# Kernel tuning notes

Hardware: AMD Instinct MI355X
Metric: run time of the kernel (lower is better)

The kernel has to match this reference:

```python
import jax, jax.numpy as jnp
import numpy as np

EPS = 1e-5
EXTEND_SCOPE = 1.0

def conv2d(x, w, b, pad):
    out = jax.lax.conv_general_dilated(x, w, (1, 1), [(pad, pad), (pad, pad)],
                                       dimension_numbers=('NCHW', 'OIHW', 'NCHW'))
    return out + b[None, :, None, None]

def group_norm(x, groups, gamma, beta):
    B, C, H, W = x.shape
    xg = x.reshape(B, groups, -1)
    mu = xg.mean(-1, keepdims=True)
    var = xg.var(-1, keepdims=True)
    xn = ((xg - mu) * jax.lax.rsqrt(var + EPS)).reshape(B, C, H, W)
    return xn * gamma[None, :, None, None] + beta[None, :, None, None]

def bilinear_sample(feat, y, x):
    # feat [B,C,H,W]; y,x pixel coords [B,Ho,Wo]; zeros padding, align_corners=True
    B, C, H, W = feat.shape
    flat = feat.reshape(B, C, H * W)
    y0 = jnp.floor(y); x0 = jnp.floor(x)
    wy = (y - y0)[:, None]; wx = (x - x0)[:, None]  # [B,1,Ho,Wo]
    y0i = y0.astype(jnp.int32); x0i = x0.astype(jnp.int32)
    Ho, Wo = y.shape[1], y.shape[2]
    def gather(yi, xi):
        valid = ((yi >= 0) & (yi < H) & (xi >= 0) & (xi < W)).astype(feat.dtype)[:, None]
        idx = (jnp.clip(yi, 0, H - 1) * W + jnp.clip(xi, 0, W - 1)).reshape(B, -1)
        g = jax.vmap(lambda f, i: f[:, i])(flat, idx).reshape(B, C, Ho, Wo)
        return g * valid
    g00 = gather(y0i, x0i)
    g01 = gather(y0i, x0i + 1)
    g10 = gather(y0i + 1, x0i)
    g11 = gather(y0i + 1, x0i + 1)
    return g00 * (1 - wy) * (1 - wx) + g01 * (1 - wy) * wx + g10 * wy * (1 - wx) + g11 * wy * wx

def setup_inputs() -> dict:
    key = jax.random.key(0)
    ks = jax.random.split(key, 4)
    B, C, H, W, K, O = 4, 64, 128, 128, 9, 64
    return {
        'x': jax.random.normal(ks[0], (B, C, H, W), jnp.float32),
        'w_off': jax.random.normal(ks[1], (K, C, 3, 3), jnp.float32) * 0.05,
        'b_off': jnp.zeros((K,), jnp.float32),
        'w_theta': jax.random.normal(ks[2], (K, C, 5, 5), jnp.float32) * 0.05,
        'b_theta': jnp.zeros((K,), jnp.float32),
        'gn_off_g': jnp.ones((K,), jnp.float32),
        'gn_off_b': jnp.zeros((K,), jnp.float32),
        'gn_th_g': jnp.ones((K,), jnp.float32),
        'gn_th_b': jnp.zeros((K,), jnp.float32),
        'w_strip': jax.random.normal(ks[3], (O, C, K, 1), jnp.float32) * 0.05,
        'b_strip': jnp.zeros((O,), jnp.float32),
        'gn_out_g': jnp.ones((O,), jnp.float32),
        'gn_out_b': jnp.zeros((O,), jnp.float32),
    }

def reference(x, w_off, b_off, w_theta, b_theta, gn_off_g, gn_off_b,
              gn_th_g, gn_th_b, w_strip, b_strip, gn_out_g, gn_out_b):
    B, C, H, W = x.shape
    K = w_off.shape[0]
    center = K // 2
    off = jnp.tanh(group_norm(conv2d(x, w_off, b_off, 1), 3, gn_off_g, gn_off_b))       # [B,K,H,W]
    th = jnp.arctan(group_norm(conv2d(x, w_theta, b_theta, 2), 3, gn_th_g, gn_th_b))    # [B,K,H,W]
    k = jnp.arange(K)
    s = (k - center).astype(x.dtype)[None, :, None, None]   # signed kernel offset
    m = center + jnp.abs(k - center)                        # mirror index (uses theta/offset at center+|i|)
    th_m = th[:, m]; off_m = off[:, m]                      # [B,K,H,W]
    is_center = (k == center)[None, :, None, None]
    y_off = jnp.where(is_center, 0.0, s * jnp.tan(th_m) + off_m * jnp.cos(th_m))
    x_off = jnp.where(is_center, 0.0, s - jnp.sin(th_m) * off_m)
    y_new = jnp.arange(H, dtype=x.dtype)[None, None, :, None] + s + EXTEND_SCOPE * y_off
    x_new = jnp.arange(W, dtype=x.dtype)[None, None, None, :] + s + EXTEND_SCOPE * x_off
    # rearrange 'b k h w -> b (h k) w'
    y_map = y_new.transpose(0, 2, 1, 3).reshape(B, H * K, W)
    x_map = x_new.transpose(0, 2, 1, 3).reshape(B, H * K, W)
    # clamp to valid range; scale to [-1,1] + align_corners=True grid_sample is identity in pixel space
    y_map = jnp.clip(y_map, 0.0, float(H - 1))
    x_map = jnp.clip(x_map, 0.0, float(W - 1))
    deformed = bilinear_sample(x, y_map, x_map)             # [B,C,K*H,W]
    d = deformed.reshape(B, C, H, K, W)
    out = jnp.einsum('bchkw,ock->bohw', d, w_strip[..., 0]) + b_strip[None, :, None, None]
    O = w_strip.shape[0]
    out = jax.nn.relu(group_norm(out, O // 4, gn_out_g, gn_out_b))
    return out
```

## Files before the change

### kernel.cpp

```cpp
#include <hip/hip_runtime.h>
#include <math.h>


typedef short v8s __attribute__((ext_vector_type(8)));
typedef float v4f __attribute__((ext_vector_type(4)));

__device__ __forceinline__ float fast_tanh(float a) {
    float aa = fabsf(a);
    float e = __expf(2.f * aa);
    float t = 1.f - 2.f / (e + 1.f);
    return copysignf(t, a);
}

__global__ __launch_bounds__(256) void k_pack(
    const float* __restrict__ w_strip, short* __restrict__ w_pack)
{
    int idx = blockIdx.x * 256 + threadIdx.x;
    int j    = idx & 7;
    int lane = (idx >> 3) & 63;
    int kk   = (idx >> 9) & 1;
    int wv   = (idx >> 10) & 3;
    int k    = idx >> 12;
    int c = (kk << 5) + ((lane >> 4) << 3) + j;
    int o = (wv << 4) + (lane & 15);
    union { short s; __bf16 h; } u;
    u.h = (__bf16)w_strip[(o * 64 + c) * 9 + k];
    w_pack[idx] = u.s;
}

__global__ __launch_bounds__(256, 8) void k_conv(
    const float* __restrict__ x,
    const float* __restrict__ w_off, const float* __restrict__ b_off,
    const float* __restrict__ w_th,  const float* __restrict__ b_th,
    float* __restrict__ off_raw, float* __restrict__ th_raw)
{
    __shared__ float tile[20][20];
    const int t  = threadIdx.x;
    const int tx = t & 15, ty = t >> 4;
    const int z  = blockIdx.z;
    const int b  = z >> 3, sp = z & 7;
    const int c0 = sp << 3;
    const int h0 = blockIdx.y << 4, w0 = blockIdx.x << 4;

    float accO[9], accT[9];
#pragma unroll
    for (int k = 0; k < 9; ++k) { accO[k] = 0.f; accT[k] = 0.f; }

    for (int ci = 0; ci < 8; ++ci) {
        const int c = c0 + ci;
        __syncthreads();
        const float* xp = x + (((b << 6) + c) << 14);
        for (int e = t; e < 400; e += 256) {
            int r = e / 20, cc = e - r * 20;
            int hh = h0 + r - 2, ww = w0 + cc - 2;
            tile[r][cc] = (hh >= 0 && hh < 128 && ww >= 0 && ww < 128)
                            ? xp[(hh << 7) + ww] : 0.f;
        }
        __syncthreads();

        float win[5][5];
#pragma unroll
        for (int i = 0; i < 5; ++i)
#pragma unroll
            for (int j = 0; j < 5; ++j)
                win[i][j] = tile[ty + i][tx + j];

#pragma unroll
        for (int k = 0; k < 9; ++k) {
            const float* wo = w_off + (size_t)((k << 6) + c) * 9;
            float a = accO[k];
#pragma unroll
            for (int i = 0; i < 3; ++i)
#pragma unroll
                for (int j = 0; j < 3; ++j)
                    a = fmaf(win[i + 1][j + 1], wo[i * 3 + j], a);
            accO[k] = a;

            const float* wt = w_th + (size_t)((k << 6) + c) * 25;
            float bb = accT[k];
#pragma unroll
            for (int i = 0; i < 5; ++i)
#pragma unroll
                for (int j = 0; j < 5; ++j)
                    bb = fmaf(win[i][j], wt[i * 5 + j], bb);
            accT[k] = bb;
        }
    }

    const int pix = ((h0 + ty) << 7) + (w0 + tx);
#pragma unroll
    for (int k = 0; k < 9; ++k) {
        float vo = accO[k] + (sp == 0 ? b_off[k] : 0.f);
        float vt = accT[k] + (sp == 0 ? b_th[k]  : 0.f);
        atomicAdd(&off_raw[((b * 9 + k) << 14) + pix], vo);
        atomicAdd(&th_raw [((b * 9 + k) << 14) + pix], vt);
    }
}

__global__ __launch_bounds__(256) void k_stats(
    const float* __restrict__ off_raw, const float* __restrict__ th_raw,
    float* __restrict__ stats)
{
    const int id  = blockIdx.x;
    const int arr = id >= 36;
    const int rem = id - arr * 36;
    const float4* src = (const float4*)((arr ? th_raw : off_raw) + (rem << 14));

    float s1 = 0.f, s2 = 0.f;
    for (int i = threadIdx.x; i < 4096; i += 256) {
        float4 v = src[i];
        s1 += v.x + v.y + v.z + v.w;
        s2 += v.x * v.x + v.y * v.y + v.z * v.z + v.w * v.w;
    }
#pragma unroll
    for (int d = 32; d; d >>= 1) { s1 += __shfl_down(s1, d, 64); s2 += __shfl_down(s2, d, 64); }

    __shared__ float ls1[4], ls2[4];
    const int wv = threadIdx.x >> 6;
    if ((threadIdx.x & 63) == 0) { ls1[wv] = s1; ls2[wv] = s2; }
    __syncthreads();
    if (threadIdx.x == 0) {
        float a = ls1[0] + ls1[1] + ls1[2] + ls1[3];
        float q = ls2[0] + ls2[1] + ls2[2] + ls2[3];
        stats[arr * 72 + rem]      = a;
        stats[arr * 72 + 36 + rem] = q;
    }
}

__global__ __launch_bounds__(256) void k_sample_strip(
    const float* __restrict__ x,
    const float* __restrict__ off_raw, const float* __restrict__ th_raw,
    const float* __restrict__ stats,
    const float* __restrict__ g_off, const float* __restrict__ be_off,
    const float* __restrict__ g_th,  const float* __restrict__ be_th,
    const short* __restrict__ w_pack, const float* __restrict__ b_strip,
    float* __restrict__ out)
{
    __shared__ __align__(16) short smem[64 * 64];
    const int t    = threadIdx.x;
    const int lane = t & 63;
    const int wv   = __builtin_amdgcn_readfirstlane(t >> 6);
    const int bid  = blockIdx.x;
    const int blk  = ((bid & 7) << 7) + (bid >> 3);
    const int b    = blk >> 8;
    const int pix0 = (blk & 255) << 6;
    const int p    = pix0 + lane;
    const int h    = p >> 7, w = p & 127;
    const int i15  = lane & 15, lg = lane >> 4;

    float muO[3], isO[3], muT[3], isT[3];
    const float inv_cnt = 1.f / (3.f * 16384.f);
#pragma unroll
    for (int g = 0; g < 3; ++g) {
        float s = 0.f, q = 0.f;
#pragma unroll
        for (int j = 0; j < 3; ++j) { s += stats[b * 9 + 3 * g + j]; q += stats[36 + b * 9 + 3 * g + j]; }
        float mu = s * inv_cnt;
        muO[g] = mu; isO[g] = rsqrtf(fmaxf(q * inv_cnt - mu * mu, 0.f) + 1e-5f);
        s = 0.f; q = 0.f;
#pragma unroll
        for (int j = 0; j < 3; ++j) { s += stats[72 + b * 9 + 3 * g + j]; q += stats[108 + b * 9 + 3 * g + j]; }
        mu = s * inv_cnt;
        muT[g] = mu; isT[g] = rsqrtf(fmaxf(q * inv_cnt - mu * mu, 0.f) + 1e-5f);
    }

    const float* xb = x + ((size_t)((b << 6) + (wv << 4)) << 14);

    v4f acc[4];
#pragma unroll
    for (int n = 0; n < 4; ++n) acc[n] = (v4f)0.f;

    for (int k = 0; k < 9; ++k) {
        float v[16];
        if (k == 4) {
#pragma unroll
            for (int ci = 0; ci < 16; ++ci) v[ci] = xb[(ci << 14) + p];
        } else {
            const int s = k - 4;
            const int m = 4 + (s < 0 ? -s : s);
            const int g = m / 3;
            float z = (th_raw[((b * 9 + m) << 14) + p] - muT[g]) * isT[g] * g_th[m] + be_th[m];
            float f = fast_tanh((off_raw[((b * 9 + m) << 14) + p] - muO[g]) * isO[g] * g_off[m] + be_off[m]);
            float r = rsqrtf(1.f + z * z);
            float fs = (float)s;
            float yy = (float)h + fs + fs * z + f * r;
            float xx = (float)w + fs + fs - z * r * f;
            yy = fminf(fmaxf(yy, 0.f), 127.f);
            xx = fminf(fmaxf(xx, 0.f), 127.f);
            int y0 = min((int)yy, 126);
            int x0 = min((int)xx, 126);
            float wy = yy - (float)y0;
            float wx = xx - (float)x0;
            const float* base = xb + (y0 << 7) + x0;
#pragma unroll
            for (int ci = 0; ci < 16; ++ci) {
                const float* q = base + (ci << 14);
                float2 r0 = *(const float2*)q;
                float2 r1 = *(const float2*)(q + 128);
                float lo = fmaf(wx, r0.y - r0.x, r0.x);
                float hi = fmaf(wx, r1.y - r1.x, r1.x);
                v[ci] = fmaf(wy, hi - lo, lo);
            }
        }

        union { v8s s8; __bf16 hh[8]; } u0, u1;
#pragma unroll
        for (int ci = 0; ci < 8; ++ci) { u0.hh[ci] = (__bf16)v[ci]; u1.hh[ci] = (__bf16)v[ci + 8]; }
        *(v8s*)&smem[(lane << 6) + ((((wv << 1) + 0) + lane) & 7) * 8] = u0.s8;
        *(v8s*)&smem[(lane << 6) + ((((wv << 1) + 1) + lane) & 7) * 8] = u1.s8;
        __syncthreads();

        const short* wpk = w_pack + (((k << 2) + wv) << 10) + (lane << 3);
        v8s a0 = *(const v8s*)wpk;
        v8s a1 = *(const v8s*)(wpk + 512);

#pragma unroll
        for (int n = 0; n < 4; ++n) {
            int r = (n << 4) + i15;
            v8s b0 = *(const v8s*)&smem[(r << 6) + (((lg    ) + r) & 7) * 8];
            v8s b1 = *(const v8s*)&smem[(r << 6) + (((lg + 4) + r) & 7) * 8];
            acc[n] = __builtin_amdgcn_mfma_f32_16x16x32_bf16(a0, b0, acc[n], 0, 0, 0);
            acc[n] = __builtin_amdgcn_mfma_f32_16x16x32_bf16(a1, b1, acc[n], 0, 0, 0);
        }
        __syncthreads();
    }

#pragma unroll
    for (int r = 0; r < 4; ++r) {
        int o = (wv << 4) + (lg << 2) + r;
        float bias = b_strip[o];
        float* op = out + ((size_t)((b << 6) + o) << 14) + pix0 + i15;
#pragma unroll
        for (int n = 0; n < 4; ++n)
            op[n << 4] = acc[n][r] + bias;
    }
}

__global__ __launch_bounds__(256) void k_stats_out(
    const float* __restrict__ out, float* __restrict__ out_stats)
{
    const int bo = blockIdx.x;
    const float4* src = (const float4*)(out + ((size_t)bo << 14));
    float s1 = 0.f, s2 = 0.f;
    for (int i = threadIdx.x; i < 4096; i += 256) {
        float4 v = src[i];
        s1 += v.x + v.y + v.z + v.w;
        s2 += v.x * v.x + v.y * v.y + v.z * v.z + v.w * v.w;
    }
#pragma unroll
    for (int d = 32; d; d >>= 1) { s1 += __shfl_down(s1, d, 64); s2 += __shfl_down(s2, d, 64); }

    __shared__ float ls1[4], ls2[4];
    const int wv = threadIdx.x >> 6;
    if ((threadIdx.x & 63) == 0) { ls1[wv] = s1; ls2[wv] = s2; }
    __syncthreads();
    if (threadIdx.x == 0) {
        out_stats[bo]       = ls1[0] + ls1[1] + ls1[2] + ls1[3];
        out_stats[256 + bo] = ls2[0] + ls2[1] + ls2[2] + ls2[3];
    }
}

__global__ __launch_bounds__(256) void k_gn_out(
    float* __restrict__ out, const float* __restrict__ out_stats,
    const float* __restrict__ gg, const float* __restrict__ gb)
{
    const float inv_cnt = 1.f / (4.f * 16384.f);
    const int n4 = 1 << 20;
    for (int idx = blockIdx.x * 256 + threadIdx.x; idx < n4; idx += gridDim.x * 256) {
        int flat = idx << 2;
        int ch = (flat >> 14) & 63;
        int b  = flat >> 20;
        int cb = (b << 6) + ((ch >> 2) << 2);
        float s = out_stats[cb] + out_stats[cb + 1] + out_stats[cb + 2] + out_stats[cb + 3];
        float q = out_stats[256 + cb] + out_stats[256 + cb + 1] + out_stats[256 + cb + 2] + out_stats[256 + cb + 3];
        float mu   = s * inv_cnt;
        float istd = rsqrtf(fmaxf(q * inv_cnt - mu * mu, 0.f) + 1e-5f);
        float ga = gg[ch] * istd;
        float be = gb[ch] - mu * ga;
        float4 v = *reinterpret_cast<float4*>(out + flat);
        v.x = fmaxf(fmaf(v.x, ga, be), 0.f);
        v.y = fmaxf(fmaf(v.y, ga, be), 0.f);
        v.z = fmaxf(fmaf(v.z, ga, be), 0.f);
        v.w = fmaxf(fmaf(v.w, ga, be), 0.f);
        *reinterpret_cast<float4*>(out + flat) = v;
    }
}

extern "C" void kernel_launch(void* const* d_in, const int* in_sizes, int n_in,
                              void* d_out, int out_size, void* d_ws, size_t ws_size,
                              hipStream_t stream)
{
    const float* x       = (const float*)d_in[0];
    const float* w_off   = (const float*)d_in[1];
    const float* b_off   = (const float*)d_in[2];
    const float* w_th    = (const float*)d_in[3];
    const float* b_th    = (const float*)d_in[4];
    const float* g_off   = (const float*)d_in[5];
    const float* be_off  = (const float*)d_in[6];
    const float* g_th    = (const float*)d_in[7];
    const float* be_th   = (const float*)d_in[8];
    const float* w_strip = (const float*)d_in[9];
    const float* b_strip = (const float*)d_in[10];
    const float* gg      = (const float*)d_in[11];
    const float* gb      = (const float*)d_in[12];

    float* out       = (float*)d_out;
    float* ws        = (float*)d_ws;
    float* off_raw   = ws;
    float* th_raw    = ws + 589824;
    float* stats     = ws + 1179648;
    float* out_stats = ws + 1179792;
    short* w_pack    = (short*)(ws + 1180304);

    hipMemsetAsync(ws, 0, (size_t)1179648 * sizeof(float), stream);

    k_pack<<<144, 256, 0, stream>>>(w_strip, w_pack);
    dim3 g1(8, 8, 32);
    k_conv<<<g1, 256, 0, stream>>>(x, w_off, b_off, w_th, b_th, off_raw, th_raw);
    k_stats<<<72, 256, 0, stream>>>(off_raw, th_raw, stats);
    k_sample_strip<<<1024, 256, 0, stream>>>(x, off_raw, th_raw, stats,
                                             g_off, be_off, g_th, be_th,
                                             w_pack, b_strip, out);
    k_stats_out<<<256, 256, 0, stream>>>(out, out_stats);
    k_gn_out<<<2048, 256, 0, stream>>>(out, out_stats, gg, gb);
}
```

Baseline: 187.4 us.

## Transpose input to channels-last for vectorized bilinear gathers in strip kernel

Adds a transpose kernel that writes x into a channels-last workspace buffer. A new sampling kernel then gathers each bilinear corner as contiguous float4 loads across channels, using 32-pixel tiles, double-buffered LDS and more blocks. The conv kernel is also changed to stage two input channels per LDS tile load. The cost is an extra full-tensor transpose pass and a fallback path that depends on the workspace size.

```diff
diff --git a/kernel.cpp b/kernel.cpp
--- a/kernel.cpp
+++ b/kernel.cpp
@@ -28,13 +28,39 @@
     w_pack[idx] = u.s;
 }
 
+__global__ __launch_bounds__(256) void k_tr(
+    const float* __restrict__ x, float* __restrict__ xt)
+{
+    __shared__ float l[64][65];
+    const int t    = threadIdx.x;
+    const int lane = t & 63;
+    const int wv   = t >> 6;
+    const int b    = blockIdx.x >> 8;
+    const int pix0 = (blockIdx.x & 255) << 6;
+
+#pragma unroll
+    for (int it = 0; it < 16; ++it) {
+        int c = (wv << 4) + it;
+        l[lane][c] = x[(((size_t)(b << 6) + c) << 14) + pix0 + lane];
+    }
+    __syncthreads();
+#pragma unroll
+    for (int it = 0; it < 4; ++it) {
+        int idx = (it << 8) + t;
+        int p  = idx >> 4;
+        int c4 = (idx & 15) << 2;
+        float4 v = { l[p][c4], l[p][c4 + 1], l[p][c4 + 2], l[p][c4 + 3] };
+        *(float4*)(xt + (((size_t)(b << 14) + pix0 + p) << 6) + c4) = v;
+    }
+}
+
 __global__ __launch_bounds__(256, 8) void k_conv(
     const float* __restrict__ x,
     const float* __restrict__ w_off, const float* __restrict__ b_off,
     const float* __restrict__ w_th,  const float* __restrict__ b_th,
     float* __restrict__ off_raw, float* __restrict__ th_raw)
 {
-    __shared__ float tile[20][20];
+    __shared__ float tile[2][20][20];
     const int t  = threadIdx.x;
     const int tx = t & 15, ty = t >> 4;
     const int z  = blockIdx.z;
@@ -46,44 +72,49 @@
 #pragma unroll
     for (int k = 0; k < 9; ++k) { accO[k] = 0.f; accT[k] = 0.f; }
 
-    for (int ci = 0; ci < 8; ++ci) {
-        const int c = c0 + ci;
+    for (int rci = 0; rci < 4; ++rci) {
         __syncthreads();
-        const float* xp = x + (((b << 6) + c) << 14);
-        for (int e = t; e < 400; e += 256) {
-            int r = e / 20, cc = e - r * 20;
+        for (int e = t; e < 800; e += 256) {
+            int ci2 = e >= 400;
+            int ee = e - (ci2 ? 400 : 0);
+            int r = ee / 20, cc = ee - r * 20;
             int hh = h0 + r - 2, ww = w0 + cc - 2;
-            tile[r][cc] = (hh >= 0 && hh < 128 && ww >= 0 && ww < 128)
-                            ? xp[(hh << 7) + ww] : 0.f;
+            const float* xp = x + (((size_t)(b << 6) + c0 + (rci << 1) + ci2) << 14);
+            tile[ci2][r][cc] = (hh >= 0 && hh < 128 && ww >= 0 && ww < 128)
+                                 ? xp[(hh << 7) + ww] : 0.f;
         }
         __syncthreads();
 
-        float win[5][5];
-#pragma unroll
-        for (int i = 0; i < 5; ++i)
-#pragma unroll
-            for (int j = 0; j < 5; ++j)
-                win[i][j] = tile[ty + i][tx + j];
-
-#pragma unroll
-        for (int k = 0; k < 9; ++k) {
-            const float* wo = w_off + (size_t)((k << 6) + c) * 9;
-            float a = accO[k];
-#pragma unroll
-            for (int i = 0; i < 3; ++i)
-#pragma unroll
-                for (int j = 0; j < 3; ++j)
-                    a = fmaf(win[i + 1][j + 1], wo[i * 3 + j], a);
-            accO[k] = a;
-
-            const float* wt = w_th + (size_t)((k << 6) + c) * 25;
-            float bb = accT[k];
+#pragma unroll
+        for (int ci2 = 0; ci2 < 2; ++ci2) {
+            const int c = c0 + (rci << 1) + ci2;
+            float win[5][5];
 #pragma unroll
             for (int i = 0; i < 5; ++i)
 #pragma unroll
                 for (int j = 0; j < 5; ++j)
-                    bb = fmaf(win[i][j], wt[i * 5 + j], bb);
-            accT[k] = bb;
+                    win[i][j] = tile[ci2][ty + i][tx + j];
+
+#pragma unroll
+            for (int k = 0; k < 9; ++k) {
+                const float* wo = w_off + (size_t)((k << 6) + c) * 9;
+                float a = accO[k];
+#pragma unroll
+                for (int i = 0; i < 3; ++i)
+#pragma unroll
+                    for (int j = 0; j < 3; ++j)
+                        a = fmaf(win[i + 1][j + 1], wo[i * 3 + j], a);
+                accO[k] = a;
+
+                const float* wt = w_th + (size_t)((k << 6) + c) * 25;
+                float bb = accT[k];
+#pragma unroll
+                for (int i = 0; i < 5; ++i)
+#pragma unroll
+                    for (int j = 0; j < 5; ++j)
+                        bb = fmaf(win[i][j], wt[i * 5 + j], bb);
+                accT[k] = bb;
+            }
         }
     }
 
@@ -120,14 +151,138 @@
     if ((threadIdx.x & 63) == 0) { ls1[wv] = s1; ls2[wv] = s2; }
     __syncthreads();
     if (threadIdx.x == 0) {
-        float a = ls1[0] + ls1[1] + ls1[2] + ls1[3];
-        float q = ls2[0] + ls2[1] + ls2[2] + ls2[3];
-        stats[arr * 72 + rem]      = a;
-        stats[arr * 72 + 36 + rem] = q;
-    }
-}
-
-__global__ __launch_bounds__(256) void k_sample_strip(
+        stats[arr * 72 + rem]      = ls1[0] + ls1[1] + ls1[2] + ls1[3];
+        stats[arr * 72 + 36 + rem] = ls2[0] + ls2[1] + ls2[2] + ls2[3];
+    }
+}
+
+__global__ __launch_bounds__(256, 8) void k_sample_strip2(
+    const float* __restrict__ xt,
+    const float* __restrict__ off_raw, const float* __restrict__ th_raw,
+    const float* __restrict__ stats,
+    const float* __restrict__ g_off, const float* __restrict__ be_off,
+    const float* __restrict__ g_th,  const float* __restrict__ be_th,
+    const short* __restrict__ w_pack, const float* __restrict__ b_strip,
+    float* __restrict__ out)
+{
+    __shared__ __align__(16) short smem[2][2048];
+    const int t    = threadIdx.x;
+    const int lane = t & 63;
+    const int wv   = __builtin_amdgcn_readfirstlane(t >> 6);
+    const int bid  = blockIdx.x;
+    const int blk  = ((bid & 7) << 8) + (bid >> 3);
+    const int b    = blk >> 9;
+    const int pix0 = (blk & 511) << 5;
+    const int l32  = lane & 31;
+    const int q    = lane >> 5;
+    const int p_img = pix0 + l32;
+    const int h    = p_img >> 7, w = p_img & 127;
+    const int i15  = lane & 15, lg = lane >> 4;
+    const int c0   = (wv << 4) + (q << 3);
+    const int cb   = (wv << 1) + q;
+
+    float muO[3], isO[3], muT[3], isT[3];
+    const float inv_cnt = 1.f / (3.f * 16384.f);
+#pragma unroll
+    for (int g = 0; g < 3; ++g) {
+        float s = 0.f, qq = 0.f;
+#pragma unroll
+        for (int j = 0; j < 3; ++j) { s += stats[b * 9 + 3 * g + j]; qq += stats[36 + b * 9 + 3 * g + j]; }
+        float mu = s * inv_cnt;
+        muO[g] = mu; isO[g] = rsqrtf(fmaxf(qq * inv_cnt - mu * mu, 0.f) + 1e-5f);
+        s = 0.f; qq = 0.f;
+#pragma unroll
+        for (int j = 0; j < 3; ++j) { s += stats[72 + b * 9 + 3 * g + j]; qq += stats[108 + b * 9 + 3 * g + j]; }
+        mu = s * inv_cnt;
+        muT[g] = mu; isT[g] = rsqrtf(fmaxf(qq * inv_cnt - mu * mu, 0.f) + 1e-5f);
+    }
+
+    const float* xtb = xt + ((size_t)(b << 14) << 6);
+
+    v4f acc[2];
+    acc[0] = (v4f)0.f; acc[1] = (v4f)0.f;
+    int cur = 0;
+
+    for (int k = 0; k < 9; ++k) {
+        float vv[8];
+        if (k == 4) {
+            const float* src = xtb + ((size_t)p_img << 6) + c0;
+            float4 A = *(const float4*)src;
+            float4 Bv = *(const float4*)(src + 4);
+            vv[0] = A.x;  vv[1] = A.y;  vv[2] = A.z;  vv[3] = A.w;
+            vv[4] = Bv.x; vv[5] = Bv.y; vv[6] = Bv.z; vv[7] = Bv.w;
+        } else {
+            const int s = k - 4;
+            const int m = 4 + (s < 0 ? -s : s);
+            const int g = m / 3;
+            float z = (th_raw[((b * 9 + m) << 14) + p_img] - muT[g]) * isT[g] * g_th[m] + be_th[m];
+            float f = fast_tanh((off_raw[((b * 9 + m) << 14) + p_img] - muO[g]) * isO[g] * g_off[m] + be_off[m]);
+            float r = rsqrtf(1.f + z * z);
+            float fs = (float)s;
+            float yy = (float)h + fs + fs * z + f * r;
+            float xx = (float)w + fs + fs - z * r * f;
+            yy = fminf(fmaxf(yy, 0.f), 127.f);
+            xx = fminf(fmaxf(xx, 0.f), 127.f);
+            int y0 = min((int)yy, 126);
+            int x0 = min((int)xx, 126);
+            float wy = yy - (float)y0;
+            float wx = xx - (float)x0;
+            const float* base = xtb + ((size_t)((y0 << 7) + x0) << 6) + c0;
+#pragma unroll
+            for (int hf = 0; hf < 2; ++hf) {
+                const float* bp = base + (hf << 2);
+                float4 c00 = *(const float4*)bp;
+                float4 c01 = *(const float4*)(bp + 64);
+                float4 c10 = *(const float4*)(bp + 8192);
+                float4 c11 = *(const float4*)(bp + 8256);
+                float tx0 = fmaf(wx, c01.x - c00.x, c00.x);
+                float ty0 = fmaf(wx, c01.y - c00.y, c00.y);
+                float tz0 = fmaf(wx, c01.z - c00.z, c00.z);
+                float tw0 = fmaf(wx, c01.w - c00.w, c00.w);
+                float bx0 = fmaf(wx, c11.x - c10.x, c10.x);
+                float by0 = fmaf(wx, c11.y - c10.y, c10.y);
+                float bz0 = fmaf(wx, c11.z - c10.z, c10.z);
+                float bw0 = fmaf(wx, c11.w - c10.w, c10.w);
+                vv[hf * 4 + 0] = fmaf(wy, bx0 - tx0, tx0);
+                vv[hf * 4 + 1] = fmaf(wy, by0 - ty0, ty0);
+                vv[hf * 4 + 2] = fmaf(wy, bz0 - tz0, tz0);
+                vv[hf * 4 + 3] = fmaf(wy, bw0 - tw0, tw0);
+            }
+        }
+
+        union { v8s s8; __bf16 hh[8]; } u;
+#pragma unroll
+        for (int j = 0; j < 8; ++j) u.hh[j] = (__bf16)vv[j];
+        *(v8s*)&smem[cur][((cb << 5) + l32) << 3] = u.s8;
+        __syncthreads();
+
+        const short* wpk = w_pack + (((k << 2) + wv) << 10) + (lane << 3);
+        v8s a0 = *(const v8s*)wpk;
+        v8s a1 = *(const v8s*)(wpk + 512);
+
+#pragma unroll
+        for (int n = 0; n < 2; ++n) {
+            int p16 = (n << 4) + i15;
+            v8s b0 = *(const v8s*)&smem[cur][((lg << 5) + p16) << 3];
+            v8s b1 = *(const v8s*)&smem[cur][(((lg + 4) << 5) + p16) << 3];
+            acc[n] = __builtin_amdgcn_mfma_f32_16x16x32_bf16(a0, b0, acc[n], 0, 0, 0);
+            acc[n] = __builtin_amdgcn_mfma_f32_16x16x32_bf16(a1, b1, acc[n], 0, 0, 0);
+        }
+        cur ^= 1;
+    }
+
+#pragma unroll
+    for (int r = 0; r < 4; ++r) {
+        int o = (wv << 4) + (lg << 2) + r;
+        float bias = b_strip[o];
+        float* op = out + (((size_t)(b << 6) + o) << 14) + pix0 + i15;
+#pragma unroll
+        for (int n = 0; n < 2; ++n)
+            op[n << 4] = acc[n][r] + bias;
+    }
+}
+
+__global__ __launch_bounds__(256) void k_sample_strip_old(
     const float* __restrict__ x,
     const float* __restrict__ off_raw, const float* __restrict__ th_raw,
     const float* __restrict__ stats,
@@ -165,7 +320,6 @@
     }
 
     const float* xb = x + ((size_t)((b << 6) + (wv << 4)) << 14);
-
     v4f acc[4];
 #pragma unroll
     for (int n = 0; n < 4; ++n) acc[n] = (v4f)0.f;
@@ -194,9 +348,9 @@
             const float* base = xb + (y0 << 7) + x0;
 #pragma unroll
             for (int ci = 0; ci < 16; ++ci) {
-                const float* q = base + (ci << 14);
-                float2 r0 = *(const float2*)q;
-                float2 r1 = *(const float2*)(q + 128);
+                const float* qp = base + (ci << 14);
+                float2 r0 = *(const float2*)qp;
+                float2 r1 = *(const float2*)(qp + 128);
                 float lo = fmaf(wx, r0.y - r0.x, r0.x);
                 float hi = fmaf(wx, r1.y - r1.x, r1.x);
                 v[ci] = fmaf(wy, hi - lo, lo);
@@ -311,16 +465,27 @@
     float* stats     = ws + 1179648;
     float* out_stats = ws + 1179792;
     short* w_pack    = (short*)(ws + 1180304);
+    float* xt        = ws + 1198736;
+
+    const size_t need_full = (size_t)(1198736 + 4194304) * sizeof(float);
+    const bool big = ws_size >= need_full;
 
     hipMemsetAsync(ws, 0, (size_t)1179648 * sizeof(float), stream);
 
     k_pack<<<144, 256, 0, stream>>>(w_strip, w_pack);
+    if (big) k_tr<<<1024, 256, 0, stream>>>(x, xt);
     dim3 g1(8, 8, 32);
     k_conv<<<g1, 256, 0, stream>>>(x, w_off, b_off, w_th, b_th, off_raw, th_raw);
     k_stats<<<72, 256, 0, stream>>>(off_raw, th_raw, stats);
-    k_sample_strip<<<1024, 256, 0, stream>>>(x, off_raw, th_raw, stats,
-                                             g_off, be_off, g_th, be_th,
-                                             w_pack, b_strip, out);
+    if (big) {
+        k_sample_strip2<<<2048, 256, 0, stream>>>(xt, off_raw, th_raw, stats,
+                                                  g_off, be_off, g_th, be_th,
+                                                  w_pack, b_strip, out);
+    } else {
+        k_sample_strip_old<<<1024, 256, 0, stream>>>(x, off_raw, th_raw, stats,
+                                                     g_off, be_off, g_th, be_th,
+                                                     w_pack, b_strip, out);
+    }
     k_stats_out<<<256, 256, 0, stream>>>(out, out_stats);
     k_gn_out<<<2048, 256, 0, stream>>>(out, out_stats, gg, gb);
 }
```

After: 210.7 us. 1.12x slower.
